# Optimization experiments

Measured on AMD Instinct MI355X. Metric: run time of the kernel, lower is better.

## Reference

```python
import jax, jax.numpy as jnp
import numpy as np

NUM_HEADS = 12


def setup_inputs() -> dict:
    key = jax.random.key(0)
    k1, k2, k3, k4, k5 = jax.random.split(key, 5)
    B, N, C = 64, 197, 768
    P = 10  # prefix length
    H, D = NUM_HEADS, C // NUM_HEADS
    return {
        "x": jax.random.normal(k1, (B, N, C), dtype=jnp.float32),
        "prompt": jax.random.normal(k2, (B, 2, P, H, D), dtype=jnp.float32),
        "qkv_w": jax.random.normal(k3, (3 * C, C), dtype=jnp.float32) * 0.02,
        "proj_w": jax.random.normal(k4, (C, C), dtype=jnp.float32) * 0.02,
        "proj_b": jax.random.normal(k5, (C,), dtype=jnp.float32) * 0.02,
    }


def reference(x, prompt, qkv_w, proj_w, proj_b):
    B, N, C = x.shape
    H = NUM_HEADS
    D = C // H
    scale = D ** -0.5

    # qkv projection (no bias), split into per-head q, k, v: [B, H, N, D]
    qkv = jnp.einsum("bnc,fc->bnf", x, qkv_w)              # [B, N, 3C]
    qkv = qkv.reshape(B, N, 3, H, D).transpose(2, 0, 3, 1, 4)
    q, k, v = qkv[0], qkv[1], qkv[2]

    # prompt: [B, 2, P, H, D] -> [2, B, H, P, D]; concat prefix onto k, v
    p = prompt.transpose(1, 0, 3, 2, 4)
    k = jnp.concatenate([p[0], k], axis=2)                  # [B, H, P+N, D]
    v = jnp.concatenate([p[1], v], axis=2)

    attn = jnp.einsum("bhnd,bhmd->bhnm", q, k) * scale      # [B, H, N, P+N]
    attn = jax.nn.softmax(attn, axis=-1)                    # attn_drop p=0 -> identity

    out = jnp.einsum("bhnm,bhmd->bhnd", attn, v)            # [B, H, N, D]
    out = out.transpose(0, 2, 1, 3).reshape(B, N, C)
    out = jnp.einsum("bnc,oc->bno", out, proj_w) + proj_b   # proj_drop p=0 -> identity
    return out
```

## Files before the change

kernel.cpp:

```cpp
#include <hip/hip_runtime.h>
#include <hip/hip_bf16.h>
#include <stdint.h>

#define NH 12
#define DH 64
#define CC 768
#define NTOK 197
#define PFX 10
#define MKV 207
#define BB 64
#define MROWS (BB * NTOK)
#define MPAD (99 * 128)
#define KV_PAD 208
#define KV_PAD2 224

typedef __attribute__((__ext_vector_type__(8))) short bf16x8;
typedef __attribute__((__ext_vector_type__(4))) float f32x4;

__device__ __forceinline__ ushort f2bf(float f) {
    union { float f; uint32_t u; } x; x.f = f;
    uint32_t u = x.u;
    return (ushort)((u + 0x7fffu + ((u >> 16) & 1u)) >> 16);
}

__device__ __forceinline__ void gload_lds16(const void* g, void* l) {
    __builtin_amdgcn_global_load_lds(
        (const __attribute__((address_space(1))) void*)g,
        (__attribute__((address_space(3))) void*)l, 16, 0, 0);
}

__global__ void cvt_bf16(const float* __restrict__ src, ushort* __restrict__ dst, int n4) {
    int i = blockIdx.x * 256 + threadIdx.x;
    if (i >= n4) return;
    float4 v = reinterpret_cast<const float4*>(src)[i];
    ushort4 o = make_ushort4(f2bf(v.x), f2bf(v.y), f2bf(v.z), f2bf(v.w));
    reinterpret_cast<ushort4*>(dst)[i] = o;
}

__global__ void prompt_scatter(const float* __restrict__ prompt,
                               ushort* __restrict__ kbuf, ushort* __restrict__ vt) {
    int i = blockIdx.x * 256 + threadIdx.x;
    if (i >= BB * 2 * PFX * NH * DH) return;
    int d = i & 63;
    int h = (i >> 6) % NH;
    int p = (i / (64 * NH)) % PFX;
    int s = (i / (64 * NH * PFX)) & 1;
    int b = i / (64 * NH * PFX * 2);
    ushort val = f2bf(prompt[i]);
    int bh = b * NH + h;
    if (s == 0) kbuf[(bh * KV_PAD + p) * DH + d] = val;
    else        vt[(bh * DH + d) * KV_PAD2 + p] = val;
}


#define GEMM_MAIN(A_, B_, KDIM)                                                      \
    __shared__ __align__(16) ushort Alds[128 * 32];                                  \
    __shared__ __align__(16) ushort Blds[128 * 32];                                  \
    const int tid  = threadIdx.x;                                                    \
    const int lane = tid & 63;                                                       \
    const int wave = tid >> 6;                                                       \
    const int wm = wave >> 1, wn = wave & 1;                                         \
    const int g = lane >> 4, lr = lane & 15;                                         \
    const int row0 = blockIdx.x * 128;                                               \
    const int col0 = blockIdx.y * 128;                                               \
    const int srow = lane >> 2;                                                      \
    const int scol = (lane & 3) * 8;                                                 \
    const ushort* gA0 = &(A_)[(size_t)(row0 + wave * 16 + srow) * (KDIM) + scol];    \
    const ushort* gA1 = gA0 + (size_t)64 * (KDIM);                                   \
    const ushort* gB0 = &(B_)[(size_t)(col0 + wave * 16 + srow) * (KDIM) + scol];    \
    const ushort* gB1 = gB0 + (size_t)64 * (KDIM);                                   \
    ushort* lA0 = &Alds[(wave * 16) * 32];                                           \
    ushort* lA1 = &Alds[(64 + wave * 16) * 32];                                      \
    ushort* lB0 = &Blds[(wave * 16) * 32];                                           \
    ushort* lB1 = &Blds[(64 + wave * 16) * 32];                                      \
    f32x4 acc[4][4] = {};                                                            \
    for (int k0 = 0; k0 < (KDIM); k0 += 32) {                                        \
        gload_lds16(gA0 + k0, lA0);                                                  \
        gload_lds16(gA1 + k0, lA1);                                                  \
        gload_lds16(gB0 + k0, lB0);                                                  \
        gload_lds16(gB1 + k0, lB1);                                                  \
        __syncthreads();     \
        bf16x8 af[4], bfr[4];                                                        \
        _Pragma("unroll")                                                            \
        for (int i = 0; i < 4; ++i)                                                  \
            af[i] = *reinterpret_cast<const bf16x8*>(&Alds[(wm * 64 + i * 16 + lr) * 32 + g * 8]); \
        _Pragma("unroll")                                                            \
        for (int i = 0; i < 4; ++i)                                                  \
            bfr[i] = *reinterpret_cast<const bf16x8*>(&Blds[(wn * 64 + i * 16 + lr) * 32 + g * 8]); \
        _Pragma("unroll")                                                            \
        for (int mi = 0; mi < 4; ++mi)                                               \
            _Pragma("unroll")                                                        \
            for (int ni = 0; ni < 4; ++ni)                                           \
                acc[mi][ni] = __builtin_amdgcn_mfma_f32_16x16x32_bf16(af[mi], bfr[ni], acc[mi][ni], 0, 0, 0); \
        __syncthreads();                                                             \
    }

__global__ __launch_bounds__(256) void gemm_qkv(const ushort* __restrict__ A,
                                                const ushort* __restrict__ Bw,
                                                ushort* __restrict__ qbuf,
                                                ushort* __restrict__ kbuf,
                                                ushort* __restrict__ vt) {
    GEMM_MAIN(A, Bw, CC)
    #pragma unroll
    for (int ni = 0; ni < 4; ++ni) {
        int f = col0 + wn * 64 + ni * 16 + lr;
        int s   = f / CC;
        int rem = f - s * CC;
        int h = rem >> 6, d = rem & 63;
        #pragma unroll
        for (int mi = 0; mi < 4; ++mi) {
            #pragma unroll
            for (int rr = 0; rr < 4; ++rr) {
                int r = row0 + wm * 64 + mi * 16 + g * 4 + rr;
                if (r >= MROWS) continue;
                int b = r / NTOK;
                int n = r - b * NTOK;
                ushort val = f2bf(acc[mi][ni][rr]);
                int bh = b * NH + h;
                if (s == 0)      qbuf[(bh * KV_PAD + n) * DH + d] = val;
                else if (s == 1) kbuf[(bh * KV_PAD + n + PFX) * DH + d] = val;
                else             vt[(bh * DH + d) * KV_PAD2 + n + PFX] = val;
            }
        }
    }
}

__global__ __launch_bounds__(256) void gemm_proj(const ushort* __restrict__ A,
                                                 const ushort* __restrict__ Bw,
                                                 const float* __restrict__ bias,
                                                 float* __restrict__ out) {
    GEMM_MAIN(A, Bw, CC)
    #pragma unroll
    for (int ni = 0; ni < 4; ++ni) {
        int o = col0 + wn * 64 + ni * 16 + lr;
        float bs = bias[o];
        #pragma unroll
        for (int mi = 0; mi < 4; ++mi) {
            #pragma unroll
            for (int rr = 0; rr < 4; ++rr) {
                int r = row0 + wm * 64 + mi * 16 + g * 4 + rr;
                if (r >= MROWS) continue;
                out[(size_t)r * CC + o] = acc[mi][ni][rr] + bs;
            }
        }
    }
}

__global__ __launch_bounds__(64) void attn(const ushort* __restrict__ qbuf,
                                           const ushort* __restrict__ kbuf,
                                           const ushort* __restrict__ vt,
                                           ushort* __restrict__ aout) {
    __shared__ __align__(16) ushort Plds[16][232];
    const int lane = threadIdx.x;
    const int g = lane >> 4, lr = lane & 15;
    const int qt = blockIdx.x;
    const int bh = blockIdx.y;
    const int b = bh / NH;
    const int h = bh - b * NH;
    const ushort* Q  = qbuf + (size_t)bh * KV_PAD * DH;
    const ushort* Kb = kbuf + (size_t)bh * KV_PAD * DH;
    const ushort* V  = vt   + (size_t)bh * DH * KV_PAD2;

    bf16x8 qf[2];
    #pragma unroll
    for (int kc = 0; kc < 2; ++kc)
        qf[kc] = *reinterpret_cast<const bf16x8*>(&Q[(qt * 16 + lr) * DH + kc * 32 + g * 8]);

    f32x4 s[13];
    #pragma unroll
    for (int t = 0; t < 13; ++t) {
        f32x4 a = {};
        #pragma unroll
        for (int kc = 0; kc < 2; ++kc) {
            bf16x8 kf = *reinterpret_cast<const bf16x8*>(&Kb[(t * 16 + lr) * DH + kc * 32 + g * 8]);
            a = __builtin_amdgcn_mfma_f32_16x16x32_bf16(kf, qf[kc], a, 0, 0, 0);
        }
        s[t] = a;
    }

    float m = -1e30f;
    #pragma unroll
    for (int t = 0; t < 13; ++t) {
        #pragma unroll
        for (int rr = 0; rr < 4; ++rr) {
            int kv = t * 16 + g * 4 + rr;
            float v = (kv < MKV) ? s[t][rr] : -1e30f;
            s[t][rr] = v;
            m = fmaxf(m, v);
        }
    }
    m = fmaxf(m, __shfl_xor(m, 16));
    m = fmaxf(m, __shfl_xor(m, 32));

    const float cs = 0.125f * 1.4426950408889634f;
    float sum = 0.f;
    #pragma unroll
    for (int t = 0; t < 13; ++t) {
        #pragma unroll
        for (int rr = 0; rr < 4; ++rr) {
            float p = exp2f((s[t][rr] - m) * cs);
            s[t][rr] = p;
            sum += p;
        }
    }
    sum += __shfl_xor(sum, 16);
    sum += __shfl_xor(sum, 32);
    float inv = 1.0f / sum;

    {
        int row = lane >> 2;
        int col = 208 + (lane & 3) * 4;
        *reinterpret_cast<ushort4*>(&Plds[row][col]) = make_ushort4(0, 0, 0, 0);
    }
    #pragma unroll
    for (int t = 0; t < 13; ++t) {
        #pragma unroll
        for (int rr = 0; rr < 4; ++rr)
            Plds[lr][t * 16 + g * 4 + rr] = f2bf(s[t][rr] * inv);
    }
    __syncthreads();

    const int q = qt * 16 + lr;
    #pragma unroll
    for (int dt = 0; dt < 4; ++dt) {
        f32x4 o = {};
        #pragma unroll
        for (int kc = 0; kc < 7; ++kc) {
            bf16x8 vf = *reinterpret_cast<const bf16x8*>(&V[(dt * 16 + lr) * KV_PAD2 + kc * 32 + g * 8]);
            bf16x8 pf = *reinterpret_cast<const bf16x8*>(&Plds[lr][kc * 32 + g * 8]);
            o = __builtin_amdgcn_mfma_f32_16x16x32_bf16(vf, pf, o, 0, 0, 0);
        }
        if (q < NTOK) {
            ushort4 st = make_ushort4(f2bf(o[0]), f2bf(o[1]), f2bf(o[2]), f2bf(o[3]));
            int r = b * NTOK + q;
            *reinterpret_cast<ushort4*>(&aout[(size_t)r * CC + h * 64 + dt * 16 + g * 4]) = st;
        }
    }
}

extern "C" void kernel_launch(void* const* d_in, const int* in_sizes, int n_in,
                              void* d_out, int out_size, void* d_ws, size_t ws_size,
                              hipStream_t stream) {
    const float* x      = (const float*)d_in[0];
    const float* prompt = (const float*)d_in[1];
    const float* qkv_w  = (const float*)d_in[2];
    const float* proj_w = (const float*)d_in[3];
    const float* proj_b = (const float*)d_in[4];
    float* out = (float*)d_out;

    char* ws = (char*)d_ws;
    ushort* Xb = (ushort*)(ws + 0);
    ushort* Wq = (ushort*)(ws + 19464192);
    ushort* Wp = (ushort*)(ws + 23003136);
    ushort* qb = (ushort*)(ws + 24182784);
    ushort* kb = (ushort*)(ws + 44630016);
    ushort* vt = (ushort*)(ws + 65077248);
    ushort* ao = (ushort*)(ws + 87097344);

    cvt_bf16<<<dim3((MROWS * CC / 4 + 255) / 256), 256, 0, stream>>>(x, Xb, MROWS * CC / 4);
    cvt_bf16<<<dim3((3 * CC * CC / 4 + 255) / 256), 256, 0, stream>>>(qkv_w, Wq, 3 * CC * CC / 4);
    cvt_bf16<<<dim3((CC * CC / 4 + 255) / 256), 256, 0, stream>>>(proj_w, Wp, CC * CC / 4);
    prompt_scatter<<<dim3((BB * 2 * PFX * NH * DH + 255) / 256), 256, 0, stream>>>(prompt, kb, vt);

    gemm_qkv<<<dim3(99, 18), 256, 0, stream>>>(Xb, Wq, qb, kb, vt);
    attn<<<dim3(13, BB * NH), 64, 0, stream>>>(qb, kb, vt, ao);
    gemm_proj<<<dim3(99, 6), 256, 0, stream>>>(ao, Wp, proj_b, out);
}
```

Baseline: 314.6 us.

## Double-buffer LDS tiles in bf16 GEMM main loop to overlap loads with MFMA

Splits the GEMM macro into stage and compute pieces and allocates two LDS buffers for A and B. The loop is unrolled by two so the next K-slice is prefetched into the alternate buffer while MFMAs run on the current one. This hides global-to-LDS latency and cuts one barrier per K step. In exchange it doubles LDS use per block, which may lower occupancy, and it assumes KDIM is a multiple of 64.

Result: no change. 315.5 us (+0.3%).

```diff
diff --git a/kernel.cpp b/kernel.cpp
--- a/kernel.cpp
+++ b/kernel.cpp
@@ -53,9 +53,11 @@
 }
 
 
-#define GEMM_MAIN(A_, B_, KDIM)                                                      \
-    __shared__ __align__(16) ushort Alds[128 * 32];                                  \
-    __shared__ __align__(16) ushort Blds[128 * 32];                                  \
+#define GEMM_PRE(A_, B_, KDIM)                                                       \
+    __shared__ __align__(16) ushort Alds0[128 * 32];                                 \
+    __shared__ __align__(16) ushort Blds0[128 * 32];                                 \
+    __shared__ __align__(16) ushort Alds1[128 * 32];                                 \
+    __shared__ __align__(16) ushort Blds1[128 * 32];                                 \
     const int tid  = threadIdx.x;                                                    \
     const int lane = tid & 63;                                                       \
     const int wave = tid >> 6;                                                       \
@@ -69,29 +71,40 @@
     const ushort* gA1 = gA0 + (size_t)64 * (KDIM);                                   \
     const ushort* gB0 = &(B_)[(size_t)(col0 + wave * 16 + srow) * (KDIM) + scol];    \
     const ushort* gB1 = gB0 + (size_t)64 * (KDIM);                                   \
-    ushort* lA0 = &Alds[(wave * 16) * 32];                                           \
-    ushort* lA1 = &Alds[(64 + wave * 16) * 32];                                      \
-    ushort* lB0 = &Blds[(wave * 16) * 32];                                           \
-    ushort* lB1 = &Blds[(64 + wave * 16) * 32];                                      \
-    f32x4 acc[4][4] = {};                                                            \
-    for (int k0 = 0; k0 < (KDIM); k0 += 32) {                                        \
-        gload_lds16(gA0 + k0, lA0);                                                  \
-        gload_lds16(gA1 + k0, lA1);                                                  \
-        gload_lds16(gB0 + k0, lB0);                                                  \
-        gload_lds16(gB1 + k0, lB1);                                                  \
-        __syncthreads();     \
+    f32x4 acc[4][4] = {};
+
+#define GEMM_STAGE(AB, BB_, KOFF)                                                    \
+    gload_lds16(gA0 + (KOFF), &(AB)[(wave * 16) * 32]);                              \
+    gload_lds16(gA1 + (KOFF), &(AB)[(64 + wave * 16) * 32]);                         \
+    gload_lds16(gB0 + (KOFF), &(BB_)[(wave * 16) * 32]);                             \
+    gload_lds16(gB1 + (KOFF), &(BB_)[(64 + wave * 16) * 32]);
+
+#define GEMM_COMPUTE(AB, BB_)                                                        \
+    {                                                                                \
         bf16x8 af[4], bfr[4];                                                        \
         _Pragma("unroll")                                                            \
         for (int i = 0; i < 4; ++i)                                                  \
-            af[i] = *reinterpret_cast<const bf16x8*>(&Alds[(wm * 64 + i * 16 + lr) * 32 + g * 8]); \
+            af[i] = *reinterpret_cast<const bf16x8*>(&(AB)[(wm * 64 + i * 16 + lr) * 32 + g * 8]); \
         _Pragma("unroll")                                                            \
         for (int i = 0; i < 4; ++i)                                                  \
-            bfr[i] = *reinterpret_cast<const bf16x8*>(&Blds[(wn * 64 + i * 16 + lr) * 32 + g * 8]); \
+            bfr[i] = *reinterpret_cast<const bf16x8*>(&(BB_)[(wn * 64 + i * 16 + lr) * 32 + g * 8]); \
         _Pragma("unroll")                                                            \
         for (int mi = 0; mi < 4; ++mi)                                               \
             _Pragma("unroll")                                                        \
             for (int ni = 0; ni < 4; ++ni)                                           \
                 acc[mi][ni] = __builtin_amdgcn_mfma_f32_16x16x32_bf16(af[mi], bfr[ni], acc[mi][ni], 0, 0, 0); \
+    }
+
+#define GEMM_MAIN(A_, B_, KDIM)                                                      \
+    GEMM_PRE(A_, B_, KDIM)                                                           \
+    GEMM_STAGE(Alds0, Blds0, 0)                                                      \
+    __syncthreads();                                                                 \
+    for (int k0 = 0; k0 < (KDIM); k0 += 64) {                                        \
+        GEMM_STAGE(Alds1, Blds1, k0 + 32)                                            \
+        GEMM_COMPUTE(Alds0, Blds0)                                                   \
+        __syncthreads();                                                             \
+        if (k0 + 64 < (KDIM)) { GEMM_STAGE(Alds0, Blds0, k0 + 64) }                  \
+        GEMM_COMPUTE(Alds1, Blds1)                                                   \
         __syncthreads();                                                             \
     }
 
```
